# Optimization experiments

Hardware: AMD Instinct MI355X
Metric: run time of the kernel (lower is better)

Reference implementation:

```python
import jax, jax.numpy as jnp
import numpy as np

N, C, H, K = 32768, 128, 4, 16
D = C // H  # head_dim = 32


def setup_inputs() -> dict:
    key = jax.random.key(0)
    ks = jax.random.split(key, 8)
    feats = jax.random.normal(ks[0], (N, C), dtype=jnp.float32)
    coords = jax.random.normal(ks[1], (N, 3), dtype=jnp.float32)
    knn_idx = jax.random.randint(ks[2], (N, K), 0, N, dtype=jnp.int64)
    s = 0.02
    Wq = jax.random.normal(ks[3], (C, C), dtype=jnp.float32) * s
    Wk = jax.random.normal(ks[4], (C, C), dtype=jnp.float32) * s
    Wv = jax.random.normal(ks[5], (C, C), dtype=jnp.float32) * s
    Wo = jax.random.normal(ks[6], (C, C), dtype=jnp.float32) * s
    bo = jnp.zeros((C,), dtype=jnp.float32)
    return {"feats": feats, "coords": coords, "knn_idx": knn_idx,
            "Wq": Wq, "Wk": Wk, "Wv": Wv, "Wo": Wo, "bo": bo}


def reference(feats, coords, knn_idx, Wq, Wk, Wv, Wo, bo):
    # coords only feeds the kNN search (precomputed as knn_idx)
    n, c = feats.shape
    q = (feats @ Wq.T).reshape(n, H, D)          # [N,H,D]
    k = (feats @ Wk.T).reshape(n, H, D)          # [N,H,D]
    v = (feats @ Wv.T).reshape(n, H, D)          # [N,H,D]
    kn = k[knn_idx]                               # gather -> [N,K,H,D]
    vn = v[knn_idx]                               # gather -> [N,K,H,D]
    scores = jnp.einsum('nhd,nkhd->nhk', q, kn) / jnp.sqrt(jnp.float32(D))
    w = jax.nn.softmax(scores, axis=-1)           # softmax over K neighbors
    out = jnp.einsum('nhk,nkhd->nhd', w, vn).reshape(n, c)
    return out @ Wo.T + bo
```

## Files before the change

kernel.cpp:

```cpp
#include <hip/hip_runtime.h>

#define NPTS 32768
#define C 128
#define KNBR 16

typedef __attribute__((ext_vector_type(8))) short short8;
typedef __attribute__((ext_vector_type(4))) float floatx4;
typedef __attribute__((ext_vector_type(4))) int intx4;

__device__ __forceinline__ ushort f2b(float f) {
    union { float f; uint u; } x; x.f = f;
    uint r = (x.u + 0x7fffu + ((x.u >> 16) & 1u)) >> 16;
    return (ushort)r;
}
__device__ __forceinline__ ushort f2h(float f) {
    union { _Float16 h; ushort u; } x; x.h = (_Float16)f; return x.u;
}
__device__ __forceinline__ float h2f(ushort u) {
    union { ushort u; _Float16 h; } x; x.u = u; return (float)x.h;
}

__global__ __launch_bounds__(256) void prep_all(
    const float* __restrict__ feats, const float* __restrict__ Wq,
    const float* __restrict__ Wk, const float* __restrict__ Wv,
    const float* __restrict__ Wo,
    ushort* __restrict__ feats_b, ushort* __restrict__ wfq,
    ushort* __restrict__ wfk, ushort* __restrict__ wfv, ushort* __restrict__ wfo)
{
    const int b = blockIdx.x, tid = threadIdx.x;
    if (b < 2048) {
        const size_t i = (size_t)b * 2048 + (size_t)tid * 8;
        float4 v0 = *(const float4*)(feats + i);
        float4 v1 = *(const float4*)(feats + i + 4);
        intx4 o;
        o.x = (int)((uint)f2b(v0.x) | ((uint)f2b(v0.y) << 16));
        o.y = (int)((uint)f2b(v0.z) | ((uint)f2b(v0.w) << 16));
        o.z = (int)((uint)f2b(v1.x) | ((uint)f2b(v1.y) << 16));
        o.w = (int)((uint)f2b(v1.z) | ((uint)f2b(v1.w) << 16));
        *(intx4*)(feats_b + i) = o;
        return;
    }
    const int wb = b - 2048;
    const int wsel = wb >> 3;
    const int tg = (wb & 7) * 256 + tid;
    const int colblk = tg >> 8;
    const int rem = tg & 255;
    const int kk = rem >> 6, kb = (rem >> 4) & 3, fr = rem & 15;
    const int col = colblk * 16 + fr;
    const int kbase = (kk * 4 + kb) * 8;

    const float* src = (wsel == 0) ? Wq : (wsel == 1) ? Wk : (wsel == 2) ? Wv : Wo;
    ushort* dst = (wsel == 0) ? wfq : (wsel == 1) ? wfk : (wsel == 2) ? wfv : wfo;

    ushort tmp[8];
#pragma unroll
    for (int e = 0; e < 8; ++e) tmp[e] = f2b(src[(size_t)col * 128 + kbase + e]);
    intx4 o;
    o.x = (int)((uint)tmp[0] | ((uint)tmp[1] << 16));
    o.y = (int)((uint)tmp[2] | ((uint)tmp[3] << 16));
    o.z = (int)((uint)tmp[4] | ((uint)tmp[5] << 16));
    o.w = (int)((uint)tmp[6] | ((uint)tmp[7] << 16));
    *(intx4*)(dst + (size_t)tg * 8) = o;
}

__global__ __launch_bounds__(256) void qkv_gemm(
    const ushort* __restrict__ A,
    const ushort* __restrict__ wfq, const ushort* __restrict__ wfk,
    const ushort* __restrict__ wfv,
    unsigned char* __restrict__ q8, unsigned char* __restrict__ kv8,
    ushort* __restrict__ scpack, float* __restrict__ qscale)
{
    __shared__ ushort ldsA[32 * 128];
    __shared__ float rmax[4][32];
    const int tid = threadIdx.x, lane = tid & 63, wid = tid >> 6;
    const int r0 = blockIdx.x * 32, sel = blockIdx.y;
    const ushort* WF = (sel == 0) ? wfq : (sel == 1) ? wfk : wfv;

#pragma unroll
    for (int it = 0; it < 2; ++it) {
        const int f = it * 256 + tid;
        const int row = f >> 4, slot = f & 15;
        intx4 v = *(const intx4*)(A + (size_t)r0 * 128 + (size_t)f * 8);
        *(intx4*)(ldsA + ((row * 16 + (slot ^ (row & 7))) * 8)) = v;
    }
    __syncthreads();

    const int fr = lane & 15, kb = lane >> 4;

    short8 af[2][4];
#pragma unroll
    for (int i = 0; i < 2; ++i)
#pragma unroll
        for (int kk = 0; kk < 4; ++kk) {
            const int row = i * 16 + fr;
            const int slot = kk * 4 + kb;
            af[i][kk] = *(const short8*)(ldsA + ((row * 16 + (slot ^ (row & 7))) * 8));
        }

    floatx4 acc[2][2];
#pragma unroll
    for (int i = 0; i < 2; ++i)
#pragma unroll
        for (int j = 0; j < 2; ++j) acc[i][j] = (floatx4){0.f, 0.f, 0.f, 0.f};

#pragma unroll
    for (int kk = 0; kk < 4; ++kk) {
        short8 bf[2];
#pragma unroll
        for (int j = 0; j < 2; ++j)
            bf[j] = *(const short8*)(WF + ((size_t)(wid * 2 + j) * 256 + kk * 64 + lane) * 8);
#pragma unroll
        for (int i = 0; i < 2; ++i)
#pragma unroll
            for (int j = 0; j < 2; ++j)
                acc[i][j] = __builtin_amdgcn_mfma_f32_16x16x32_bf16(af[i][kk], bf[j], acc[i][j], 0, 0, 0);
    }

    float mx[2][4];
#pragma unroll
    for (int i = 0; i < 2; ++i)
#pragma unroll
        for (int r = 0; r < 4; ++r) {
            float m = fmaxf(fabsf(acc[i][0][r]), fabsf(acc[i][1][r]));
            m = fmaxf(m, __shfl_xor(m, 1));
            m = fmaxf(m, __shfl_xor(m, 2));
            m = fmaxf(m, __shfl_xor(m, 4));
            m = fmaxf(m, __shfl_xor(m, 8));
            mx[i][r] = m;
        }
    if (fr == 0) {
#pragma unroll
        for (int i = 0; i < 2; ++i)
#pragma unroll
            for (int r = 0; r < 4; ++r)
                rmax[wid][i * 16 + kb * 4 + r] = mx[i][r];
    }
    __syncthreads();

    const int boff = (wid * 8 + (fr >> 1)) * 4;
#pragma unroll
    for (int i = 0; i < 2; ++i)
#pragma unroll
        for (int r = 0; r < 4; ++r) {
            const int lr = i * 16 + kb * 4 + r;
            const int nn = r0 + lr;
            float comb = fmaxf(rmax[0][lr], rmax[1][lr]);
            comb = fmaxf(comb, rmax[2][lr]);
            comb = fmaxf(comb, rmax[3][lr]);
            comb = fmaxf(comb, 1e-20f);
            const float qs = 127.f / comb;
            int b0 = __float2int_rn(acc[i][0][r] * qs);
            int b1 = __float2int_rn(acc[i][1][r] * qs);
            uint u16 = (uint)(b0 & 0xff) | ((uint)(b1 & 0xff) << 8);
            uint o16 = __shfl_xor(u16, 1);
            if (wid == 0 && fr == 0) {
                if (sel == 0)      qscale[nn] = comb * (1.f / 127.f);
                else if (sel == 1) scpack[(size_t)nn * 2]     = f2h(comb * (1.f / 127.f));
                else               scpack[(size_t)nn * 2 + 1] = f2h(comb * (1.f / 127.f));
            }
            if (!(fr & 1)) {
                const uint word = u16 | (o16 << 16);
                if (sel == 0)      *(uint*)(q8  + (size_t)nn * 128 + boff) = word;
                else if (sel == 1) *(uint*)(kv8 + (size_t)nn * 256 + boff) = word;
                else               *(uint*)(kv8 + (size_t)nn * 256 + 128 + boff) = word;
            }
        }
}

__global__ __launch_bounds__(256, 6) void attn_kernel(
    const unsigned char* __restrict__ q8, const unsigned char* __restrict__ kv8,
    const ushort* __restrict__ scpack, const float* __restrict__ qscale,
    const int* __restrict__ knn, ushort* __restrict__ attn_p)
{
    const int tid = threadIdx.x;
    const int lane = tid & 63;
    const int wp = __builtin_amdgcn_readfirstlane(tid >> 6);
    const int n = blockIdx.x * 4 + wp;

    const int kk = lane >> 2, h = lane & 3;
    const int nb4 = knn[(size_t)n * KNBR + kk];
    const int* kr = knn + (size_t)n * KNBR;

    const unsigned char* krow = kv8 + (size_t)nb4 * 256 + h * 32;
    intx4 k0 = *(const intx4*)(krow);
    intx4 k1 = *(const intx4*)(krow + 16);
    const unsigned char* qrow = q8 + (size_t)n * 128 + h * 32;
    intx4 qq0 = *(const intx4*)(qrow);
    intx4 qq1 = *(const intx4*)(qrow + 16);
    const uint scp = *(const uint*)(scpack + (size_t)nb4 * 2);

    ushort vsh[KNBR];
#pragma unroll
    for (int j = 0; j < KNBR; ++j) {
        const int nbv = kr[j];
        vsh[j] = *(const ushort*)(kv8 + (size_t)nbv * 256 + 128 + lane * 2);
    }

    const float qs6 = qscale[n] * 0.17677669529663687f;

    int dp = 0;
#if __has_builtin(__builtin_amdgcn_sdot4)
#pragma unroll
    for (int i = 0; i < 4; ++i) dp = __builtin_amdgcn_sdot4(qq0[i], k0[i], dp, false);
#pragma unroll
    for (int i = 0; i < 4; ++i) dp = __builtin_amdgcn_sdot4(qq1[i], k1[i], dp, false);
#else
#pragma unroll
    for (int i = 0; i < 4; ++i) {
        uint a = (uint)qq0[i], b = (uint)k0[i];
        dp += (int)(signed char)(a) * (int)(signed char)(b)
            + (int)(signed char)(a >> 8) * (int)(signed char)(b >> 8)
            + (int)(signed char)(a >> 16) * (int)(signed char)(b >> 16)
            + (int)(signed char)(a >> 24) * (int)(signed char)(b >> 24);
        a = (uint)qq1[i]; b = (uint)k1[i];
        dp += (int)(signed char)(a) * (int)(signed char)(b)
            + (int)(signed char)(a >> 8) * (int)(signed char)(b >> 8)
            + (int)(signed char)(a >> 16) * (int)(signed char)(b >> 16)
            + (int)(signed char)(a >> 24) * (int)(signed char)(b >> 24);
    }
#endif

    const float ksc = h2f((ushort)(scp & 0xffff));
    const float vsc = h2f((ushort)(scp >> 16));
    const float sc = (float)dp * ksc * qs6;

    float mxv = sc;
    mxv = fmaxf(mxv, __shfl_xor(mxv, 4));
    mxv = fmaxf(mxv, __shfl_xor(mxv, 8));
    mxv = fmaxf(mxv, __shfl_xor(mxv, 16));
    mxv = fmaxf(mxv, __shfl_xor(mxv, 32));
    const float e = __expf(sc - mxv);
    float sm = e;
    sm += __shfl_xor(sm, 4);
    sm += __shfl_xor(sm, 8);
    sm += __shfl_xor(sm, 16);
    sm += __shfl_xor(sm, 32);
    const float wgt = e * vsc / sm;

    const int h2v = lane >> 4;
    float a0 = 0.f, a1 = 0.f;
#pragma unroll
    for (int j = 0; j < KNBR; ++j) {
        const float w2 = __shfl(wgt, j * 4 + h2v);
        const ushort u = vsh[j];
        a0 += w2 * (float)(signed char)(u & 0xff);
        a1 += w2 * (float)(signed char)(u >> 8);
    }
    const int cb = 32 * (lane >> 4) + (lane & 15);
    attn_p[(size_t)n * 128 + cb]      = f2b(a0);
    attn_p[(size_t)n * 128 + cb + 16] = f2b(a1);
}

__global__ __launch_bounds__(256) void out_gemm(
    const ushort* __restrict__ A, const ushort* __restrict__ wfo,
    const float* __restrict__ bias, float* __restrict__ out)
{
    __shared__ ushort ldsA[32 * 128];
    const int tid = threadIdx.x, lane = tid & 63, wid = tid >> 6;
    const int r0 = blockIdx.x * 32;

#pragma unroll
    for (int it = 0; it < 2; ++it) {
        const int f = it * 256 + tid;
        const int row = f >> 4, slot = f & 15;
        intx4 v = *(const intx4*)(A + (size_t)r0 * 128 + (size_t)f * 8);
        *(intx4*)(ldsA + ((row * 16 + (slot ^ (row & 7))) * 8)) = v;
    }
    __syncthreads();

    const int fr = lane & 15, kb = lane >> 4;

    short8 af[2][4];
#pragma unroll
    for (int i = 0; i < 2; ++i)
#pragma unroll
        for (int kk = 0; kk < 4; ++kk) {
            const int row = i * 16 + fr;
            const int slot = kk * 4 + kb;
            af[i][kk] = *(const short8*)(ldsA + ((row * 16 + (slot ^ (row & 7))) * 8));
        }

    floatx4 acc[2][2];
#pragma unroll
    for (int i = 0; i < 2; ++i)
#pragma unroll
        for (int j = 0; j < 2; ++j) acc[i][j] = (floatx4){0.f, 0.f, 0.f, 0.f};

#pragma unroll
    for (int kk = 0; kk < 4; ++kk) {
        short8 bf[2];
#pragma unroll
        for (int j = 0; j < 2; ++j)
            bf[j] = *(const short8*)(wfo + ((size_t)(wid * 2 + j) * 256 + kk * 64 + lane) * 8);
#pragma unroll
        for (int i = 0; i < 2; ++i)
#pragma unroll
            for (int j = 0; j < 2; ++j)
                acc[i][j] = __builtin_amdgcn_mfma_f32_16x16x32_bf16(af[i][kk], bf[j], acc[i][j], 0, 0, 0);
    }

#pragma unroll
    for (int j = 0; j < 2; ++j) {
        const int col = wid * 32 + j * 16 + fr;
        const float bv = bias[col];
#pragma unroll
        for (int i = 0; i < 2; ++i)
#pragma unroll
            for (int r = 0; r < 4; ++r) {
                const int n = r0 + i * 16 + kb * 4 + r;
                out[(size_t)n * 128 + col] = acc[i][j][r] + bv;
            }
    }
}

extern "C" void kernel_launch(void* const* d_in, const int* in_sizes, int n_in,
                              void* d_out, int out_size, void* d_ws, size_t ws_size,
                              hipStream_t stream)
{
    const float* feats = (const float*)d_in[0];
    const int*   knn   = (const int*)d_in[2];
    const float* Wq    = (const float*)d_in[3];
    const float* Wk    = (const float*)d_in[4];
    const float* Wv    = (const float*)d_in[5];
    const float* Wo    = (const float*)d_in[6];
    const float* bo    = (const float*)d_in[7];
    float* out = (float*)d_out;

    ushort* feats_b = (ushort*)d_ws;
    ushort* attn_p  = feats_b + (size_t)NPTS * C;
    unsigned char* q8  = (unsigned char*)(attn_p + (size_t)NPTS * C);
    unsigned char* kv8 = q8 + (size_t)NPTS * 128;
    ushort* scpack = (ushort*)(kv8 + (size_t)NPTS * 256);
    float* qscale  = (float*)(scpack + (size_t)NPTS * 2);
    ushort* wfq    = (ushort*)(qscale + (size_t)NPTS);
    ushort* wfk    = wfq + 16384;
    ushort* wfv    = wfk + 16384;
    ushort* wfo    = wfv + 16384;

    prep_all<<<2080, 256, 0, stream>>>(feats, Wq, Wk, Wv, Wo,
                                       feats_b, wfq, wfk, wfv, wfo);
    qkv_gemm<<<dim3(NPTS / 32, 3), 256, 0, stream>>>(feats_b, wfq, wfk, wfv,
                                                     q8, kv8, scpack, qscale);
    attn_kernel<<<NPTS / 4, 256, 0, stream>>>(q8, kv8, scpack, qscale, knn, attn_p);
    out_gemm<<<NPTS / 32, 256, 0, stream>>>(attn_p, wfo, bo, out);
}
```

Before: 48.40 us.

## Fuse feats bf16 conversion into QKV GEMM and compute Q,K,V per block

Removes the separate feats-to-bf16 pass and its bf16 workspace round trip. qkv_gemm now loads fp32 feats directly, converts them into swizzled LDS once, and loops over the Q, K and V weights in one block instead of launching three grid columns. The A tile is read once instead of three times, at the cost of fewer blocks (a third of the previous grid) and more sequential work per block. Each projection now uses its own rmax slot.

```diff
diff --git a/kernel.cpp b/kernel.cpp
--- a/kernel.cpp
+++ b/kernel.cpp
@@ -20,29 +20,15 @@
     union { ushort u; _Float16 h; } x; x.u = u; return (float)x.h;
 }
 
-__global__ __launch_bounds__(256) void prep_all(
-    const float* __restrict__ feats, const float* __restrict__ Wq,
-    const float* __restrict__ Wk, const float* __restrict__ Wv,
-    const float* __restrict__ Wo,
-    ushort* __restrict__ feats_b, ushort* __restrict__ wfq,
-    ushort* __restrict__ wfk, ushort* __restrict__ wfv, ushort* __restrict__ wfo)
+__global__ __launch_bounds__(256) void prep_w(
+    const float* __restrict__ Wq, const float* __restrict__ Wk,
+    const float* __restrict__ Wv, const float* __restrict__ Wo,
+    ushort* __restrict__ wfq, ushort* __restrict__ wfk,
+    ushort* __restrict__ wfv, ushort* __restrict__ wfo)
 {
     const int b = blockIdx.x, tid = threadIdx.x;
-    if (b < 2048) {
-        const size_t i = (size_t)b * 2048 + (size_t)tid * 8;
-        float4 v0 = *(const float4*)(feats + i);
-        float4 v1 = *(const float4*)(feats + i + 4);
-        intx4 o;
-        o.x = (int)((uint)f2b(v0.x) | ((uint)f2b(v0.y) << 16));
-        o.y = (int)((uint)f2b(v0.z) | ((uint)f2b(v0.w) << 16));
-        o.z = (int)((uint)f2b(v1.x) | ((uint)f2b(v1.y) << 16));
-        o.w = (int)((uint)f2b(v1.z) | ((uint)f2b(v1.w) << 16));
-        *(intx4*)(feats_b + i) = o;
-        return;
-    }
-    const int wb = b - 2048;
-    const int wsel = wb >> 3;
-    const int tg = (wb & 7) * 256 + tid;
+    const int wsel = b >> 3;
+    const int tg = (b & 7) * 256 + tid;
     const int colblk = tg >> 8;
     const int rem = tg & 255;
     const int kk = rem >> 6, kb = (rem >> 4) & 3, fr = rem & 15;
@@ -64,24 +50,31 @@
 }
 
 __global__ __launch_bounds__(256) void qkv_gemm(
-    const ushort* __restrict__ A,
+    const float* __restrict__ feats,
     const ushort* __restrict__ wfq, const ushort* __restrict__ wfk,
     const ushort* __restrict__ wfv,
     unsigned char* __restrict__ q8, unsigned char* __restrict__ kv8,
     ushort* __restrict__ scpack, float* __restrict__ qscale)
 {
     __shared__ ushort ldsA[32 * 128];
-    __shared__ float rmax[4][32];
+    __shared__ float rmax[3][4][32];
     const int tid = threadIdx.x, lane = tid & 63, wid = tid >> 6;
-    const int r0 = blockIdx.x * 32, sel = blockIdx.y;
-    const ushort* WF = (sel == 0) ? wfq : (sel == 1) ? wfk : wfv;
-
-#pragma unroll
-    for (int it = 0; it < 2; ++it) {
+    const int r0 = blockIdx.x * 32;
+
+    float4 va[4];
+#pragma unroll
+    for (int it = 0; it < 4; ++it) {
         const int f = it * 256 + tid;
-        const int row = f >> 4, slot = f & 15;
-        intx4 v = *(const intx4*)(A + (size_t)r0 * 128 + (size_t)f * 8);
-        *(intx4*)(ldsA + ((row * 16 + (slot ^ (row & 7))) * 8)) = v;
+        va[it] = *(const float4*)(feats + (size_t)r0 * 128 + (size_t)f * 4);
+    }
+#pragma unroll
+    for (int it = 0; it < 4; ++it) {
+        const int f = it * 256 + tid;
+        const int row = f >> 5, slot = (f & 31) >> 1, half = f & 1;
+        uint2 o;
+        o.x = (uint)f2b(va[it].x) | ((uint)f2b(va[it].y) << 16);
+        o.y = (uint)f2b(va[it].z) | ((uint)f2b(va[it].w) << 16);
+        *(uint2*)(ldsA + (row * 16 + (slot ^ (row & 7))) * 8 + half * 4) = o;
     }
     __syncthreads();
 
@@ -94,77 +87,83 @@
         for (int kk = 0; kk < 4; ++kk) {
             const int row = i * 16 + fr;
             const int slot = kk * 4 + kb;
-            af[i][kk] = *(const short8*)(ldsA + ((row * 16 + (slot ^ (row & 7))) * 8));
+            af[i][kk] = *(const short8*)(ldsA + (row * 16 + (slot ^ (row & 7))) * 8);
         }
 
-    floatx4 acc[2][2];
-#pragma unroll
-    for (int i = 0; i < 2; ++i)
-#pragma unroll
-        for (int j = 0; j < 2; ++j) acc[i][j] = (floatx4){0.f, 0.f, 0.f, 0.f};
-
-#pragma unroll
-    for (int kk = 0; kk < 4; ++kk) {
-        short8 bf[2];
-#pragma unroll
-        for (int j = 0; j < 2; ++j)
-            bf[j] = *(const short8*)(WF + ((size_t)(wid * 2 + j) * 256 + kk * 64 + lane) * 8);
-#pragma unroll
-        for (int i = 0; i < 2; ++i)
+    const int boff = (wid * 8 + (fr >> 1)) * 4;
+
+#pragma unroll
+    for (int sel = 0; sel < 3; ++sel) {
+        const ushort* WF = (sel == 0) ? wfq : (sel == 1) ? wfk : wfv;
+
+        floatx4 acc[2][2];
+#pragma unroll
+        for (int i = 0; i < 2; ++i)
+#pragma unroll
+            for (int j = 0; j < 2; ++j) acc[i][j] = (floatx4){0.f, 0.f, 0.f, 0.f};
+
+#pragma unroll
+        for (int kk = 0; kk < 4; ++kk) {
+            short8 bf[2];
 #pragma unroll
             for (int j = 0; j < 2; ++j)
-                acc[i][j] = __builtin_amdgcn_mfma_f32_16x16x32_bf16(af[i][kk], bf[j], acc[i][j], 0, 0, 0);
-    }
-
-    float mx[2][4];
-#pragma unroll
-    for (int i = 0; i < 2; ++i)
-#pragma unroll
-        for (int r = 0; r < 4; ++r) {
-            float m = fmaxf(fabsf(acc[i][0][r]), fabsf(acc[i][1][r]));
-            m = fmaxf(m, __shfl_xor(m, 1));
-            m = fmaxf(m, __shfl_xor(m, 2));
-            m = fmaxf(m, __shfl_xor(m, 4));
-            m = fmaxf(m, __shfl_xor(m, 8));
-            mx[i][r] = m;
+                bf[j] = *(const short8*)(WF + ((size_t)(wid * 2 + j) * 256 + kk * 64 + lane) * 8);
+#pragma unroll
+            for (int i = 0; i < 2; ++i)
+#pragma unroll
+                for (int j = 0; j < 2; ++j)
+                    acc[i][j] = __builtin_amdgcn_mfma_f32_16x16x32_bf16(af[i][kk], bf[j], acc[i][j], 0, 0, 0);
         }
-    if (fr == 0) {
-#pragma unroll
-        for (int i = 0; i < 2; ++i)
-#pragma unroll
-            for (int r = 0; r < 4; ++r)
-                rmax[wid][i * 16 + kb * 4 + r] = mx[i][r];
-    }
-    __syncthreads();
-
-    const int boff = (wid * 8 + (fr >> 1)) * 4;
-#pragma unroll
-    for (int i = 0; i < 2; ++i)
-#pragma unroll
-        for (int r = 0; r < 4; ++r) {
-            const int lr = i * 16 + kb * 4 + r;
-            const int nn = r0 + lr;
-            float comb = fmaxf(rmax[0][lr], rmax[1][lr]);
-            comb = fmaxf(comb, rmax[2][lr]);
-            comb = fmaxf(comb, rmax[3][lr]);
-            comb = fmaxf(comb, 1e-20f);
-            const float qs = 127.f / comb;
-            int b0 = __float2int_rn(acc[i][0][r] * qs);
-            int b1 = __float2int_rn(acc[i][1][r] * qs);
-            uint u16 = (uint)(b0 & 0xff) | ((uint)(b1 & 0xff) << 8);
-            uint o16 = __shfl_xor(u16, 1);
-            if (wid == 0 && fr == 0) {
-                if (sel == 0)      qscale[nn] = comb * (1.f / 127.f);
-                else if (sel == 1) scpack[(size_t)nn * 2]     = f2h(comb * (1.f / 127.f));
-                else               scpack[(size_t)nn * 2 + 1] = f2h(comb * (1.f / 127.f));
+
+        float mx[2][4];
+#pragma unroll
+        for (int i = 0; i < 2; ++i)
+#pragma unroll
+            for (int r = 0; r < 4; ++r) {
+                float m = fmaxf(fabsf(acc[i][0][r]), fabsf(acc[i][1][r]));
+                m = fmaxf(m, __shfl_xor(m, 1));
+                m = fmaxf(m, __shfl_xor(m, 2));
+                m = fmaxf(m, __shfl_xor(m, 4));
+                m = fmaxf(m, __shfl_xor(m, 8));
+                mx[i][r] = m;
             }
-            if (!(fr & 1)) {
-                const uint word = u16 | (o16 << 16);
-                if (sel == 0)      *(uint*)(q8  + (size_t)nn * 128 + boff) = word;
-                else if (sel == 1) *(uint*)(kv8 + (size_t)nn * 256 + boff) = word;
-                else               *(uint*)(kv8 + (size_t)nn * 256 + 128 + boff) = word;
+        if (fr == 0) {
+#pragma unroll
+            for (int i = 0; i < 2; ++i)
+#pragma unroll
+                for (int r = 0; r < 4; ++r)
+                    rmax[sel][wid][i * 16 + kb * 4 + r] = mx[i][r];
+        }
+        __syncthreads();
+
+#pragma unroll
+        for (int i = 0; i < 2; ++i)
+#pragma unroll
+            for (int r = 0; r < 4; ++r) {
+                const int lr = i * 16 + kb * 4 + r;
+                const int nn = r0 + lr;
+                float comb = fmaxf(rmax[sel][0][lr], rmax[sel][1][lr]);
+                comb = fmaxf(comb, rmax[sel][2][lr]);
+                comb = fmaxf(comb, rmax[sel][3][lr]);
+                comb = fmaxf(comb, 1e-20f);
+                const float qs = 127.f / comb;
+                int b0 = __float2int_rn(acc[i][0][r] * qs);
+                int b1 = __float2int_rn(acc[i][1][r] * qs);
+                uint u16 = (uint)(b0 & 0xff) | ((uint)(b1 & 0xff) << 8);
+                uint o16 = __shfl_xor(u16, 1);
+                if (wid == 0 && fr == 0) {
+                    if (sel == 0)      qscale[nn] = comb * (1.f / 127.f);
+                    else if (sel == 1) scpack[(size_t)nn * 2]     = f2h(comb * (1.f / 127.f));
+                    else               scpack[(size_t)nn * 2 + 1] = f2h(comb * (1.f / 127.f));
+                }
+                if (!(fr & 1)) {
+                    const uint word = u16 | (o16 << 16);
+                    if (sel == 0)      *(uint*)(q8  + (size_t)nn * 128 + boff) = word;
+                    else if (sel == 1) *(uint*)(kv8 + (size_t)nn * 256 + boff) = word;
+                    else               *(uint*)(kv8 + (size_t)nn * 256 + 128 + boff) = word;
+                }
             }
-        }
+    }
 }
 
 __global__ __launch_bounds__(256, 6) void attn_kernel(
@@ -326,8 +325,7 @@
     const float* bo    = (const float*)d_in[7];
     float* out = (float*)d_out;
 
-    ushort* feats_b = (ushort*)d_ws;
-    ushort* attn_p  = feats_b + (size_t)NPTS * C;
+    ushort* attn_p = (ushort*)d_ws;
     unsigned char* q8  = (unsigned char*)(attn_p + (size_t)NPTS * C);
     unsigned char* kv8 = q8 + (size_t)NPTS * 128;
     ushort* scpack = (ushort*)(kv8 + (size_t)NPTS * 256);
@@ -337,10 +335,9 @@
     ushort* wfv    = wfk + 16384;
     ushort* wfo    = wfv + 16384;
 
-    prep_all<<<2080, 256, 0, stream>>>(feats, Wq, Wk, Wv, Wo,
-                                       feats_b, wfq, wfk, wfv, wfo);
-    qkv_gemm<<<dim3(NPTS / 32, 3), 256, 0, stream>>>(feats_b, wfq, wfk, wfv,
-                                                     q8, kv8, scpack, qscale);
+    prep_w<<<32, 256, 0, stream>>>(Wq, Wk, Wv, Wo, wfq, wfk, wfv, wfo);
+    qkv_gemm<<<NPTS / 32, 256, 0, stream>>>(feats, wfq, wfk, wfv,
+                                            q8, kv8, scpack, qscale);
     attn_kernel<<<NPTS / 4, 256, 0, stream>>>(q8, kv8, scpack, qscale, knn, attn_p);
     out_gemm<<<NPTS / 32, 256, 0, stream>>>(attn_p, wfo, bo, out);
 }
```

After: 50.15 us. +3.6%, slower.
